# Kernel optimization log

Measured on AMD Instinct MI355X. Metric: run time of the kernel, lower is better.

The kernel has to match this reference:

```python
import jax, jax.numpy as jnp
import numpy as np

K = 3   # 4D kernel size
P = 1   # padding (all 4 dims)
S = 1   # stride (all 4 dims)
DIL = 1 # dilation

def setup_inputs() -> dict:
    key = jax.random.key(0)
    k1, k2, k3 = jax.random.split(key, 3)
    x = jax.random.normal(k1, (2, 8, 16, 40, 40, 40), dtype=jnp.float32)
    # K separate Conv3d layers: weight[i] has shape [C_o, C_i, K, K, K]
    weight = jax.random.normal(k2, (K, 32, 8, K, K, K), dtype=jnp.float32) * 0.05
    bias = jax.random.normal(k3, (K, 32), dtype=jnp.float32) * 0.05
    return {"x": x, "weight": weight, "bias": bias}

def reference(x, weight, bias):
    # x: [B, C_i, T, D, H, W]; weight: [K, C_o, C_i, K, K, K]; bias: [K, C_o]
    B, Ci, T, D, H, W = x.shape
    Co = weight.shape[1]
    O = (T + 2 * P - K) // S + 1
    # Fold temporal frames into the batch dim and all K conv3d filters into
    # the output-channel dim -> a single conv3d replaces K*T launches.
    x2 = jnp.transpose(x, (0, 2, 1, 3, 4, 5)).reshape(B * T, Ci, D, H, W)
    w = weight.reshape(K * Co, Ci, K, K, K)
    y = jax.lax.conv_general_dilated(
        x2, w,
        window_strides=(S, S, S),
        padding=[(P, P)] * 3,
        rhs_dilation=(DIL, DIL, DIL),
        dimension_numbers=("NCDHW", "OIDHW", "NCDHW"),
    )  # [B*T, K*Co, Dp, Hp, Wp]
    Dp, Hp, Wp = y.shape[-3:]
    y = y.reshape(B, T, K, Co, Dp, Hp, Wp)
    # bias is added per Conv3d call, i.e. once per contributing (i, j) pair
    y = y + bias[None, None, :, :, None, None, None]
    # Temporal accumulation: out[o] = sum_i y[j = o*S + i - P, i] (skip OOB j),
    # implemented via zero-padding (padded frames contribute nothing, incl. bias).
    y_pad = jnp.pad(y, ((0, 0), (P, P), (0, 0), (0, 0), (0, 0), (0, 0), (0, 0)))
    idx = jnp.arange(O)[:, None] * S + jnp.arange(K)[None, :]  # [O, K] indices into padded T
    gathered = y_pad[:, idx, jnp.arange(K)[None, :]]  # [B, O, K, Co, Dp, Hp, Wp]
    out = gathered.sum(axis=2)  # [B, O, Co, Dp, Hp, Wp]
    return jnp.transpose(out, (0, 2, 1, 3, 4, 5))  # [B, Co, O, Dp, Hp, Wp]
```

## Files before the change

kernel.cpp:

```cpp
#include <hip/hip_runtime.h>


typedef unsigned int u32;
typedef unsigned short u16;
typedef __attribute__((ext_vector_type(8))) short short8;
typedef __attribute__((ext_vector_type(4))) float f32x4;

#define XT_OFF_BYTES 65536

__device__ __forceinline__ u32 bf16r(float f) {
    u32 u = __float_as_uint(f);
    return (u + 0x7FFFu + ((u >> 16) & 1u)) >> 16;
}

__device__ __forceinline__ void glds16(const void* g, void* l) {
    __builtin_amdgcn_global_load_lds((const __attribute__((address_space(1))) u32*)g,
                                     (__attribute__((address_space(3))) u32*)l, 16, 0, 0);
}

__global__ __launch_bounds__(256) void prep_x(const float* __restrict__ x, u16* __restrict__ xtp) {
    const int c = blockIdx.x * 256 + threadIdx.x;
    int wp = c % 42;
    int tmp = c / 42;
    const int hp = tmp % 42; tmp /= 42;
    const int dp = tmp % 42; tmp /= 42;
    const int t  = tmp % 16;
    const int b  = tmp / 16;
    const int wa = wp - 1, ha = hp - 1, da = dp - 1;
    u32 q0 = 0, q1 = 0, q2 = 0, q3 = 0;
    if ((unsigned)wa < 40u && (unsigned)ha < 40u && (unsigned)da < 40u) {
        const float* xp = x + ((b * 8) * 16 + t) * 64000 + da * 1600 + ha * 40 + wa;
        float v0 = xp[0];
        float v1 = xp[1024000];
        float v2 = xp[2048000];
        float v3 = xp[3072000];
        float v4 = xp[4096000];
        float v5 = xp[5120000];
        float v6 = xp[6144000];
        float v7 = xp[7168000];
        q0 = bf16r(v0) | (bf16r(v1) << 16);
        q1 = bf16r(v2) | (bf16r(v3) << 16);
        q2 = bf16r(v4) | (bf16r(v5) << 16);
        q3 = bf16r(v6) | (bf16r(v7) << 16);
    }
    uint4 q; q.x = q0; q.y = q1; q.z = q2; q.w = q3;
    *(uint4*)(xtp + (size_t)c * 8) = q;
}

__global__ __launch_bounds__(256) void prep_w(const float* __restrict__ wgt, u16* __restrict__ wf) {
    const int idx = blockIdx.x * 256 + threadIdx.x;
    const int kt = idx / 7168;
    const int r  = idx - kt * 7168;
    const int s2 = r >> 9;
    const int l  = (r >> 3) & 63;
    const int j  = r & 7;
    const int co = (s2 & 1) * 16 + (l & 15);
    const int k  = (s2 >> 1) * 32 + (l >> 4) * 8 + j;
    u32 v = 0;
    if (k < 216) {
        const int ci = k & 7;
        const int combo = k >> 3;
        const int kd = combo / 9;
        const int r9 = combo - kd * 9;
        const int kh = r9 / 3;
        const int kw = r9 - kh * 3;
        v = bf16r(wgt[((kt * 32 + co) * 8 + ci) * 27 + kd * 9 + kh * 3 + kw]);
    }
    wf[idx] = (u16)v;
}

__global__ __launch_bounds__(320, 4) void conv4d_mfma(
    const u16* __restrict__ xtp, const u16* __restrict__ wf,
    const float* __restrict__ bias, float* __restrict__ out)
{
    __shared__ __align__(16) u16 sWf[7168];
    __shared__ __align__(16) u16 sHalo[10080];
    __shared__ float sBsum[32];

    const int tid  = threadIdx.x;
    const int lane = tid & 63;
    const int wid  = tid >> 6;
    const int bi   = blockIdx.x;
    const int h0   = (bi % 5) * 8;
    const int d    = (bi / 5) % 40;
    const int o    = (bi / 200) % 16;
    const int b    = bi / 3200;

    if (tid < 32) {
        float s = 0.f;
        for (int kt = 0; kt < 3; ++kt) {
            int t = o + kt - 1;
            if ((unsigned)t < 16u) s += bias[kt * 32 + tid];
        }
        sBsum[tid] = s;
    }

    const int quad = lane >> 4;
    const int nl   = lane & 15;

    int hh[4], ww[4], lb[4];
#pragma unroll
    for (int tl = 0; tl < 4; ++tl) {
        int n = wid * 64 + tl * 16 + nl;
        hh[tl] = n / 40;
        ww[tl] = n - hh[tl] * 40;
        lb[tl] = (hh[tl] * 42 + ww[tl]) * 16;
    }

    int offs7[7];
#pragma unroll
    for (int s = 0; s < 7; ++s) {
        const int c0 = 4 * s;
        int O0 = (c0+0 < 27) ? (((c0+0)/9)*420 + (((c0+0)%9)/3)*42 + ((c0+0)%3)) * 16 : 0;
        int O1 = (c0+1 < 27) ? (((c0+1)/9)*420 + (((c0+1)%9)/3)*42 + ((c0+1)%3)) * 16 : 0;
        int O2 = (c0+2 < 27) ? (((c0+2)/9)*420 + (((c0+2)%9)/3)*42 + ((c0+2)%3)) * 16 : 0;
        int O3 = (c0+3 < 27) ? (((c0+3)/9)*420 + (((c0+3)%9)/3)*42 + ((c0+3)%3)) * 16 : 0;
        offs7[s] = (quad & 2) ? ((quad & 1) ? O3 : O2) : ((quad & 1) ? O1 : O0);
    }

    const f32x4 zero = {0.f, 0.f, 0.f, 0.f};
    f32x4 acc[2][4];
#pragma unroll
    for (int mt = 0; mt < 2; ++mt)
#pragma unroll
        for (int tl = 0; tl < 4; ++tl) acc[mt][tl] = zero;

#pragma unroll
    for (int kt = 0; kt < 3; ++kt) {
        const int t = o + kt - 1;
        if ((unsigned)t >= 16u) continue;

        __syncthreads();

        {
            const u16* wfg = wf + kt * 7168;
            const int jb = wid * 180;
#pragma unroll
            for (int i = 0; i < 3; ++i) {
                const int io = i * 64 + lane;
                const int j = jb + io;
                if (io < 180 && j < 896) {
                    glds16(wfg + j * 8, (char*)sWf + (jb + i * 64) * 16);
                }
            }
        }
        {
            const u16* gbase = xtp + (size_t)(b * 16 + t) * 592704 + h0 * 336;
            const int jw = wid * 252;
#pragma unroll
            for (int i = 0; i < 4; ++i) {
                const int j = jw + i * 64 + lane;
                if (i < 3 || lane < 60) {
                    const int dpp = j / 420;
                    const int r = j - dpp * 420;
                    glds16(gbase + (d + dpp) * 14112 + r * 8, (char*)sHalo + (jw + i * 64) * 16);
                }
            }
        }
        __syncthreads();

#pragma unroll
        for (int s = 0; s < 7; ++s) {
            const short8 a0 = *(const short8*)((const char*)sWf + s * 2048 + lane * 16);
            const short8 a1 = *(const short8*)((const char*)sWf + s * 2048 + 1024 + lane * 16);
            const int off = offs7[s];
#pragma unroll
            for (int tl = 0; tl < 4; ++tl) {
                const short8 bf = *(const short8*)((const char*)sHalo + lb[tl] + off);
                acc[0][tl] = __builtin_amdgcn_mfma_f32_16x16x32_bf16(a0, bf, acc[0][tl], 0, 0, 0);
                acc[1][tl] = __builtin_amdgcn_mfma_f32_16x16x32_bf16(a1, bf, acc[1][tl], 0, 0, 0);
            }
        }
    }

    const int coB = quad * 4;
    float bs[2][4];
#pragma unroll
    for (int mt = 0; mt < 2; ++mt)
#pragma unroll
        for (int reg = 0; reg < 4; ++reg) bs[mt][reg] = sBsum[mt * 16 + coB + reg];

#pragma unroll
    for (int mt = 0; mt < 2; ++mt)
#pragma unroll
        for (int tl = 0; tl < 4; ++tl) {
            const size_t base = (size_t)(((b * 32 + mt * 16 + coB) * 16 + o)) * 64000
                              + d * 1600 + (h0 + hh[tl]) * 40 + ww[tl];
#pragma unroll
            for (int reg = 0; reg < 4; ++reg)
                out[base + (size_t)reg * 1024000] = acc[mt][tl][reg] + bs[mt][reg];
        }
}

extern "C" void kernel_launch(void* const* d_in, const int* in_sizes, int n_in,
                              void* d_out, int out_size, void* d_ws, size_t ws_size,
                              hipStream_t stream)
{
    const float* x    = (const float*)d_in[0];
    const float* wgt  = (const float*)d_in[1];
    const float* bias = (const float*)d_in[2];
    float* out = (float*)d_out;
    u16* wfbuf = (u16*)d_ws;
    u16* xtp   = (u16*)((char*)d_ws + XT_OFF_BYTES);
    (void)in_sizes; (void)n_in; (void)out_size; (void)ws_size;

    prep_w<<<dim3(84),   dim3(256), 0, stream>>>(wgt, wfbuf);
    prep_x<<<dim3(9261), dim3(256), 0, stream>>>(x, xtp);
    conv4d_mfma<<<dim3(6400), dim3(320), 0, stream>>>(xtp, wfbuf, bias, out);
}
```

Measured before the change: 366.0 us.

## Read conv weights from global directly and use 4 waves with 5 tiles each

The weight staging in shared memory is removed, and each wave now loads its MFMA A operands straight from global memory, where they should be served from cache. The block shrinks from 5 to 4 waves, with each wave covering 80 output positions (5 tiles) instead of 64. That frees LDS and cuts the per-timestep copy work. The cost is more accumulator registers per thread and global-load latency inside the inner loop.

```diff
diff --git a/kernel.cpp b/kernel.cpp
--- a/kernel.cpp
+++ b/kernel.cpp
@@ -69,11 +69,10 @@
     wf[idx] = (u16)v;
 }
 
-__global__ __launch_bounds__(320, 4) void conv4d_mfma(
+__global__ __launch_bounds__(256, 4) void conv4d_mfma(
     const u16* __restrict__ xtp, const u16* __restrict__ wf,
     const float* __restrict__ bias, float* __restrict__ out)
 {
-    __shared__ __align__(16) u16 sWf[7168];
     __shared__ __align__(16) u16 sHalo[10080];
     __shared__ float sBsum[32];
 
@@ -98,13 +97,13 @@
     const int quad = lane >> 4;
     const int nl   = lane & 15;
 
-    int hh[4], ww[4], lb[4];
-#pragma unroll
-    for (int tl = 0; tl < 4; ++tl) {
-        int n = wid * 64 + tl * 16 + nl;
-        hh[tl] = n / 40;
-        ww[tl] = n - hh[tl] * 40;
-        lb[tl] = (hh[tl] * 42 + ww[tl]) * 16;
+    int lb[5];
+#pragma unroll
+    for (int tl = 0; tl < 5; ++tl) {
+        int n = wid * 80 + tl * 16 + nl;
+        int hh = n / 40;
+        int ww = n - hh * 40;
+        lb[tl] = (hh * 42 + ww) * 16;
     }
 
     int offs7[7];
@@ -119,38 +118,26 @@
     }
 
     const f32x4 zero = {0.f, 0.f, 0.f, 0.f};
-    f32x4 acc[2][4];
+    f32x4 acc[2][5];
 #pragma unroll
     for (int mt = 0; mt < 2; ++mt)
 #pragma unroll
-        for (int tl = 0; tl < 4; ++tl) acc[mt][tl] = zero;
+        for (int tl = 0; tl < 5; ++tl) acc[mt][tl] = zero;
 
 #pragma unroll
     for (int kt = 0; kt < 3; ++kt) {
         const int t = o + kt - 1;
+
+        __syncthreads();
         if ((unsigned)t >= 16u) continue;
 
-        __syncthreads();
-
-        {
-            const u16* wfg = wf + kt * 7168;
-            const int jb = wid * 180;
-#pragma unroll
-            for (int i = 0; i < 3; ++i) {
-                const int io = i * 64 + lane;
-                const int j = jb + io;
-                if (io < 180 && j < 896) {
-                    glds16(wfg + j * 8, (char*)sWf + (jb + i * 64) * 16);
-                }
-            }
-        }
         {
             const u16* gbase = xtp + (size_t)(b * 16 + t) * 592704 + h0 * 336;
-            const int jw = wid * 252;
-#pragma unroll
-            for (int i = 0; i < 4; ++i) {
+            const int jw = wid * 315;
+#pragma unroll
+            for (int i = 0; i < 5; ++i) {
                 const int j = jw + i * 64 + lane;
-                if (i < 3 || lane < 60) {
+                if (i < 4 || lane < 59) {
                     const int dpp = j / 420;
                     const int r = j - dpp * 420;
                     glds16(gbase + (d + dpp) * 14112 + r * 8, (char*)sHalo + (jw + i * 64) * 16);
@@ -159,13 +146,14 @@
         }
         __syncthreads();
 
+        const u16* wfk = wf + kt * 7168;
 #pragma unroll
         for (int s = 0; s < 7; ++s) {
-            const short8 a0 = *(const short8*)((const char*)sWf + s * 2048 + lane * 16);
-            const short8 a1 = *(const short8*)((const char*)sWf + s * 2048 + 1024 + lane * 16);
+            const short8 a0 = *(const short8*)(wfk + s * 1024 + lane * 8);
+            const short8 a1 = *(const short8*)(wfk + s * 1024 + 512 + lane * 8);
             const int off = offs7[s];
 #pragma unroll
-            for (int tl = 0; tl < 4; ++tl) {
+            for (int tl = 0; tl < 5; ++tl) {
                 const short8 bf = *(const short8*)((const char*)sHalo + lb[tl] + off);
                 acc[0][tl] = __builtin_amdgcn_mfma_f32_16x16x32_bf16(a0, bf, acc[0][tl], 0, 0, 0);
                 acc[1][tl] = __builtin_amdgcn_mfma_f32_16x16x32_bf16(a1, bf, acc[1][tl], 0, 0, 0);
@@ -183,9 +171,12 @@
 #pragma unroll
     for (int mt = 0; mt < 2; ++mt)
 #pragma unroll
-        for (int tl = 0; tl < 4; ++tl) {
+        for (int tl = 0; tl < 5; ++tl) {
+            int n = wid * 80 + tl * 16 + nl;
+            int hh = n / 40;
+            int ww = n - hh * 40;
             const size_t base = (size_t)(((b * 32 + mt * 16 + coB) * 16 + o)) * 64000
-                              + d * 1600 + (h0 + hh[tl]) * 40 + ww[tl];
+                              + d * 1600 + (h0 + hh) * 40 + ww;
 #pragma unroll
             for (int reg = 0; reg < 4; ++reg)
                 out[base + (size_t)reg * 1024000] = acc[mt][tl][reg] + bs[mt][reg];
@@ -206,5 +197,5 @@
 
     prep_w<<<dim3(84),   dim3(256), 0, stream>>>(wgt, wfbuf);
     prep_x<<<dim3(9261), dim3(256), 0, stream>>>(x, xtp);
-    conv4d_mfma<<<dim3(6400), dim3(320), 0, stream>>>(xtp, wfbuf, bias, out);
-}
+    conv4d_mfma<<<dim3(6400), dim3(256), 0, stream>>>(xtp, wfbuf, bias, out);
+}
```

Measured after the change: 366.4 us. About the same (+0.1%).
